# Optimization experiments

Measured on AMD Instinct MI355X. Metric: run time of the kernel, lower is better.

## Reference

```python
import jax, jax.numpy as jnp
import numpy as np
from jax import lax

B, T, H, L = 64, 512, 768, 9


def setup_inputs() -> dict:
    key = jax.random.key(0)
    ks = jax.random.split(key, 6)
    return {
        "seq_out": jax.random.normal(ks[0], (B, T, H), dtype=jnp.float32),
        "mask": jnp.ones((B, T), dtype=bool),
        "W_fc": jax.random.normal(ks[1], (H, L), dtype=jnp.float32) * 0.02,
        "b_fc": jax.random.normal(ks[2], (L,), dtype=jnp.float32) * 0.02,
        "start_transitions": jax.random.normal(ks[3], (L,), dtype=jnp.float32) * 0.1,
        "end_transitions": jax.random.normal(ks[4], (L,), dtype=jnp.float32) * 0.1,
        "transitions": jax.random.normal(ks[5], (L, L), dtype=jnp.float32) * 0.1,
    }


def reference(seq_out, mask, W_fc, b_fc, start_transitions, end_transitions, transitions):
    # linear head (dropout is identity at inference)
    emissions = jnp.einsum("bth,hl->btl", seq_out, W_fc) + b_fc  # (B,T,L)

    # --- Viterbi forward pass (torchcrf semantics) ---
    score0 = start_transitions + emissions[:, 0]  # (B,L)
    emis_rest = jnp.swapaxes(emissions[:, 1:], 0, 1)  # (T-1,B,L)
    mask_rest = jnp.swapaxes(mask[:, 1:], 0, 1)       # (T-1,B)

    def step(score, inp):
        emit_t, mask_t = inp
        # (B, prev L, next L)
        full = score[:, :, None] + transitions[None, :, :] + emit_t[:, None, :]
        next_score = jnp.max(full, axis=1)
        best_prev = jnp.argmax(full, axis=1)  # (B,L) best previous tag
        new_score = jnp.where(mask_t[:, None], next_score, score)
        return new_score, best_prev

    score, history = lax.scan(step, score0, (emis_rest, mask_rest))  # history: (T-1,B,L)

    last_tag = jnp.argmax(score + end_transitions, axis=1)  # (B,)

    # --- backtrace (mask is all-ones -> every sequence has full length T) ---
    def back(tag, hist_t):
        prev = jnp.take_along_axis(hist_t, tag[:, None], axis=1)[:, 0]
        return prev, tag  # emit tag at t+1, carry tag at t

    first_tag, tags_rest = lax.scan(back, last_tag, history, reverse=True)
    tags = jnp.concatenate([first_tag[:, None], jnp.swapaxes(tags_rest, 0, 1)], axis=1)
    return tags  # (B,T) int32 best tag sequence
```

## Files before the change

### kernel.cpp

```cpp
#include <hip/hip_runtime.h>
#include <stdint.h>

typedef unsigned long long u64;

#define T_SZ 512
#define H_SZ 768
#define L_SZ 9
#define KCHUNK 192
#define NINF (-__builtin_inff())

__device__ __forceinline__ float max3f(float a, float b, float c)
{
  return fmaxf(fmaxf(a, b), c);
}

__global__ __launch_bounds__(256) void emis_kernel(
    const float* __restrict__ seq, const float* __restrict__ W,
    const float* __restrict__ bfc, float* __restrict__ emis)
{
  const int tid  = threadIdx.x;
  const int lane = tid & 63;
  const int wid  = __builtin_amdgcn_readfirstlane(tid >> 6);

  const int row = blockIdx.x * 64 + lane;
  const float* x     = seq + (size_t)row * H_SZ + wid * KCHUNK;
  const float* wbase = W + (size_t)wid * KCHUNK * L_SZ;

  float acc[L_SZ];
#pragma unroll
  for (int j = 0; j < L_SZ; ++j) acc[j] = 0.f;

#pragma unroll 2
  for (int i = 0; i < KCHUNK / 4; ++i) {
    const float4 xv = *reinterpret_cast<const float4*>(x + 4 * i);
    const float* wp = wbase + 36 * i;
    float wf[36];
#pragma unroll
    for (int q = 0; q < 9; ++q)
      *reinterpret_cast<float4*>(&wf[4 * q]) =
          *reinterpret_cast<const float4*>(wp + 4 * q);
#pragma unroll
    for (int j = 0; j < L_SZ; ++j)
      acc[j] += xv.x * wf[j] + xv.y * wf[9 + j] + xv.z * wf[18 + j] + xv.w * wf[27 + j];
  }

  __shared__ float s_part[4 * 64 * L_SZ];
  {
    float* myp = s_part + (wid * 64 + lane) * L_SZ;
#pragma unroll
    for (int j = 0; j < L_SZ; ++j) myp[j] = acc[j];
  }
  __syncthreads();

  for (int o = tid; o < 64 * L_SZ; o += 256) {
    const int j = o % L_SZ;
    const float s = s_part[o] + s_part[576 + o] + s_part[1152 + o] + s_part[1728 + o];
    emis[(size_t)blockIdx.x * (64 * L_SZ) + o] = s + bfc[j];
  }
}

#define ROTI(K, v) __builtin_amdgcn_mov_dpp((v), 0x120 + (K), 0xF, 0xF, true)
#define ROTF(K, v) __int_as_float(__builtin_amdgcn_mov_dpp(__float_as_int(v), 0x120 + (K), 0xF, 0xF, true))

__device__ __forceinline__ u64 comp9(u64 a, u64 b)
{
  u64 r = 0;
#pragma unroll
  for (int x = 0; x < 9; ++x) {
    const int bx = (int)((b >> (4 * x)) & 15ull);
    const u64 ax = (a >> (bx * 4)) & 15ull;
    r |= ax << (4 * x);
  }
  return r;
}
__device__ __forceinline__ int app9(u64 f, int x) { return (int)((f >> (4 * x)) & 15ull); }

__device__ __forceinline__ u64 shfl_dn64(u64 v, int d)
{
  unsigned lo = __shfl_down((unsigned)v, d, 64);
  unsigned hi = __shfl_down((unsigned)(v >> 32), d, 64);
  return ((u64)hi << 32) | lo;
}

__global__ __launch_bounds__(256) void viterbi_kernel(
    const float* __restrict__ emis, const float* __restrict__ trans,
    const float* __restrict__ startT, const float* __restrict__ endT,
    int* __restrict__ tags)
{
  const int b   = blockIdx.x;
  const int tid = threadIdx.x;

  __shared__ __align__(16) float s_emis[T_SZ * L_SZ + 32];
  __shared__ float s_score[T_SZ * L_SZ + 8];
  __shared__ float s_T16[16 * 16];
  __shared__ unsigned char s_hist[T_SZ * L_SZ];
  __shared__ int s_last;

  {
    const float4* src = reinterpret_cast<const float4*>(emis + (size_t)b * T_SZ * L_SZ);
    float4* dst = reinterpret_cast<float4*>(s_emis);
    for (int i = tid; i < (T_SZ * L_SZ) / 4; i += 256) dst[i] = src[i];
  }
  {
    const int i = tid >> 4, j = tid & 15;
    s_T16[tid] = (i < L_SZ && j < L_SZ) ? trans[i * L_SZ + j] : NINF;
  }
  __syncthreads();

  if (tid < 16) {
    const int jj  = tid;
    const int jje = (jj < L_SZ) ? jj : (L_SZ - 1);

    float Tp[16];
    {
      int xk;
      Tp[0] = s_T16[jj * 16 + jj];
#define SETTP(K) xk = ROTI(K, jj); Tp[K] = s_T16[xk * 16 + jj];
      SETTP(1)  SETTP(2)  SETTP(3)  SETTP(4)  SETTP(5)
      SETTP(6)  SETTP(7)  SETTP(8)  SETTP(9)  SETTP(10)
      SETTP(11) SETTP(12) SETTP(13) SETTP(14) SETTP(15)
#undef SETTP
    }

    float r = (jj < L_SZ) ? (startT[jje] + s_emis[jj]) : NINF;
    s_score[jj] = r;

    float e0 = s_emis[1 * L_SZ + jje];
    float e1 = s_emis[2 * L_SZ + jje];
    const float* ep = s_emis + 3 * L_SZ + jje;
    float* sp = s_score + L_SZ + jj;

#pragma unroll 2
    for (int t = 1; t < T_SZ; ++t) {
      const float e2 = *ep; ep += L_SZ;
      float a[16];
      a[0] = r + Tp[0];
#define GATH(K) a[K] = ROTF(K, r) + Tp[K];
      GATH(1)  GATH(2)  GATH(3)  GATH(4)  GATH(5)
      GATH(6)  GATH(7)  GATH(8)  GATH(9)  GATH(10)
      GATH(11) GATH(12) GATH(13) GATH(14) GATH(15)
#undef GATH
      const float m0 = max3f(a[0], a[1], a[2]);
      const float m1 = max3f(a[3], a[4], a[5]);
      const float m2 = max3f(a[6], a[7], a[8]);
      const float m3 = max3f(a[9], a[10], a[11]);
      const float m4 = max3f(a[12], a[13], a[14]);
      const float n0 = max3f(m0, m1, m2);
      const float n1 = max3f(m3, m4, a[15]);
      r = fmaxf(n0, n1) + e0;
      *sp = r; sp += L_SZ;
      e0 = e1; e1 = e2;
    }

    const float fin = r + ((jj < L_SZ) ? endT[jje] : 0.f);
    float g[16]; int gi[16];
    g[0] = fin; gi[0] = jj;
#define GFIN(K) g[K] = ROTF(K, fin); gi[K] = ROTI(K, jj);
    GFIN(1)  GFIN(2)  GFIN(3)  GFIN(4)  GFIN(5)
    GFIN(6)  GFIN(7)  GFIN(8)  GFIN(9)  GFIN(10)
    GFIN(11) GFIN(12) GFIN(13) GFIN(14) GFIN(15)
#undef GFIN
    const float q0 = max3f(g[0], g[1], g[2]);
    const float q1 = max3f(g[3], g[4], g[5]);
    const float q2 = max3f(g[6], g[7], g[8]);
    const float q3 = max3f(g[9], g[10], g[11]);
    const float q4 = max3f(g[12], g[13], g[14]);
    const float mm = fmaxf(max3f(q0, q1, q2), max3f(q3, q4, g[15]));
    int li = 99;
#pragma unroll
    for (int k = 0; k < 16; ++k) li = min(li, (g[k] == mm) ? gi[k] : 99);
    if (jj == 0) s_last = li;
  }
  __syncthreads();

  for (int p = tid; p < (T_SZ - 1) * L_SZ; p += 256) {
    const int t = p / L_SZ + 1;
    const int j = p - (t - 1) * L_SZ;
    const float e = s_emis[t * L_SZ + j];
    const float* sp2 = s_score + (t - 1) * L_SZ;
    float ci[9];
#pragma unroll
    for (int i = 0; i < 9; ++i) ci[i] = (sp2[i] + s_T16[i * 16 + j]) + e;
    const float m = fmaxf(max3f(max3f(ci[0], ci[1], ci[2]),
                                max3f(ci[3], ci[4], ci[5]),
                                max3f(ci[6], ci[7], ci[8])), ci[8]);
    int bi = 8;
#pragma unroll
    for (int i = 8; i >= 0; --i) bi = (ci[i] == m) ? i : bi;
    s_hist[t * L_SZ + j] = (unsigned char)bi;
  }
  __syncthreads();

  if (tid < 64) {
    const u64 IDENT = 0x876543210ull;
    const int k = tid;
    const int last = s_last;

    u64 f[8];
#pragma unroll
    for (int r8 = 0; r8 < 8; ++r8) {
      const int s = 8 * k + r8;
      u64 v = 0;
#pragma unroll
      for (int x = 0; x < 9; ++x)
        v |= (u64)(s_hist[s * L_SZ + x] & 15) << (4 * x);
      f[r8] = v;
    }
    if (k == 0) f[0] = IDENT;

    u64 C = f[7];
#pragma unroll
    for (int r8 = 6; r8 >= 0; --r8) C = comp9(f[r8], C);

    u64 S = C;
#pragma unroll
    for (int d = 1; d < 64; d <<= 1) {
      u64 o = shfl_dn64(S, d);
      if (k + d > 63) o = IDENT;
      S = comp9(S, o);
    }
    u64 E = shfl_dn64(S, 1);
    if (k == 63) E = IDENT;

    int val = app9(E, last);
    int* ob = tags + b * T_SZ;
    ob[8 * k + 7] = val;
#pragma unroll
    for (int r8 = 7; r8 >= 0; --r8) {
      val = app9(f[r8], val);
      const int s = 8 * k + r8;
      if (s >= 1) ob[s - 1] = val;
    }
  }
}

extern "C" void kernel_launch(void* const* d_in, const int* in_sizes, int n_in,
                              void* d_out, int out_size, void* d_ws, size_t ws_size,
                              hipStream_t stream)
{
  const float* seq   = (const float*)d_in[0];
  const float* W     = (const float*)d_in[2];
  const float* bfc   = (const float*)d_in[3];
  const float* stT   = (const float*)d_in[4];
  const float* enT   = (const float*)d_in[5];
  const float* trans = (const float*)d_in[6];

  int*   tags = (int*)d_out;
  float* emis = (float*)d_ws;

  emis_kernel<<<(T_SZ * 64) / 64, 256, 0, stream>>>(seq, W, bfc, emis);
  viterbi_kernel<<<64, 256, 0, stream>>>(emis, trans, stT, enT, tags);
}
```

Baseline: 72.59 us.

## Stage sequence rows through padded LDS for coalesced emission GEMV loads

The emission kernel now loads 64 rows of seq_out in four 192-column chunks into a padded shared buffer. Groups of four threads read contiguous float4s, so the global loads are coalesced, where before each lane streamed its own row with a large stride. Each warp then computes a 48-column slice of every chunk from LDS. This adds extra barriers and LDS traffic, and the per-lane partial sums are still reduced through shared memory at the end.

```diff
diff --git a/kernel.cpp b/kernel.cpp
--- a/kernel.cpp
+++ b/kernel.cpp
@@ -6,7 +6,6 @@
 #define T_SZ 512
 #define H_SZ 768
 #define L_SZ 9
-#define KCHUNK 192
 #define NINF (-__builtin_inff())
 
 __device__ __forceinline__ float max3f(float a, float b, float c)
@@ -22,29 +21,48 @@
   const int lane = tid & 63;
   const int wid  = __builtin_amdgcn_readfirstlane(tid >> 6);
 
-  const int row = blockIdx.x * 64 + lane;
-  const float* x     = seq + (size_t)row * H_SZ + wid * KCHUNK;
-  const float* wbase = W + (size_t)wid * KCHUNK * L_SZ;
+  __shared__ float s_x[64 * 193];
+  __shared__ float s_part[4 * 64 * L_SZ];
+
+  const int row64 = blockIdx.x * 64;
+  const int r   = tid >> 2;
+  const int seg = tid & 3;
 
   float acc[L_SZ];
 #pragma unroll
   for (int j = 0; j < L_SZ; ++j) acc[j] = 0.f;
 
+  for (int c = 0; c < 4; ++c) {
+    __syncthreads();
+    {
+      const float* src = seq + (size_t)(row64 + r) * H_SZ + 192 * c;
+#pragma unroll
+      for (int i = 0; i < 12; ++i) {
+        const int f4 = 4 * i + seg;
+        const float4 v = *reinterpret_cast<const float4*>(src + 4 * f4);
+        float* d = &s_x[r * 193 + 4 * f4];
+        d[0] = v.x; d[1] = v.y; d[2] = v.z; d[3] = v.w;
+      }
+    }
+    __syncthreads();
+    const float* wbase = W + (size_t)(192 * c + 48 * wid) * L_SZ;
+    const float* xr = &s_x[lane * 193 + 48 * wid];
 #pragma unroll 2
-  for (int i = 0; i < KCHUNK / 4; ++i) {
-    const float4 xv = *reinterpret_cast<const float4*>(x + 4 * i);
-    const float* wp = wbase + 36 * i;
-    float wf[36];
-#pragma unroll
-    for (int q = 0; q < 9; ++q)
-      *reinterpret_cast<float4*>(&wf[4 * q]) =
-          *reinterpret_cast<const float4*>(wp + 4 * q);
-#pragma unroll
-    for (int j = 0; j < L_SZ; ++j)
-      acc[j] += xv.x * wf[j] + xv.y * wf[9 + j] + xv.z * wf[18 + j] + xv.w * wf[27 + j];
-  }
-
-  __shared__ float s_part[4 * 64 * L_SZ];
+    for (int i = 0; i < 12; ++i) {
+      const float x0 = xr[4 * i + 0], x1 = xr[4 * i + 1];
+      const float x2 = xr[4 * i + 2], x3 = xr[4 * i + 3];
+      const float* wp = wbase + 36 * i;
+      float wf[36];
+#pragma unroll
+      for (int q = 0; q < 9; ++q)
+        *reinterpret_cast<float4*>(&wf[4 * q]) =
+            *reinterpret_cast<const float4*>(wp + 4 * q);
+#pragma unroll
+      for (int j = 0; j < L_SZ; ++j)
+        acc[j] += x0 * wf[j] + x1 * wf[9 + j] + x2 * wf[18 + j] + x3 * wf[27 + j];
+    }
+  }
+
   {
     float* myp = s_part + (wid * 64 + lane) * L_SZ;
 #pragma unroll
```

Result: slower. 75.01 us (+3.3%).
